# Optimization experiments

Measured on AMD Instinct MI355X. Metric: run time of the kernel, lower is better.

The kernel has to match this reference:

```python
import jax, jax.numpy as jnp
import numpy as np

N, E, IN_DIM, H_DIM, T = 100000, 3200000, 128, 128, 5000


def gcn_conv(x, W, b, src, dst):
    """PyG GCNConv: symmetric norm with self-loops, linear transform, scatter-add."""
    n = x.shape[0]
    h = x @ W  # [N, h]
    # degree with self-loops (all edge weights = 1)
    deg = jax.ops.segment_sum(jnp.ones(src.shape[0], x.dtype), dst, num_segments=n) + 1.0
    dinv = jax.lax.rsqrt(deg)  # deg >= 1 due to self-loops
    norm = dinv[src] * dinv[dst]  # [E]
    out = jax.ops.segment_sum(h[src] * norm[:, None], dst, num_segments=n)
    out = out + h * (dinv * dinv)[:, None]  # self-loop contribution
    return out + b


def setup_inputs() -> dict:
    key = jax.random.key(0)
    ks = jax.random.split(key, 24)
    s_in = 1.0 / np.sqrt(IN_DIM)
    s_h = 1.0 / np.sqrt(H_DIM)
    return {
        "x": jax.random.normal(ks[0], (N, IN_DIM), jnp.float32),
        "edge_index": jax.random.randint(ks[1], (2, E), 0, N),
        "fake_x": jax.random.normal(ks[2], (N, IN_DIM), jnp.float32),
        "fake_edge_index": jax.random.randint(ks[3], (2, E), 0, N),
        "treat_idx": jax.random.randint(ks[4], (T,), 0, N),
        "control_idx": jax.random.randint(ks[5], (T,), 0, N),
        # GCN layer params
        "W1": jax.random.normal(ks[6], (IN_DIM, H_DIM), jnp.float32) * s_in,
        "b1": jnp.zeros((H_DIM,), jnp.float32),
        "W2": jax.random.normal(ks[7], (H_DIM, H_DIM), jnp.float32) * s_h,
        "b2": jnp.zeros((H_DIM,), jnp.float32),
        # heads
        "Wy1": jax.random.normal(ks[8], (H_DIM, 1), jnp.float32) * s_h,
        "by1": jnp.zeros((1,), jnp.float32),
        "Wy0": jax.random.normal(ks[9], (H_DIM, 1), jnp.float32) * s_h,
        "by0": jnp.zeros((1,), jnp.float32),
        "Wb": jax.random.normal(ks[10], (H_DIM, 2), jnp.float32) * s_h,
        "bb": jnp.zeros((2,), jnp.float32),
        "Wp1": jax.random.normal(ks[11], (H_DIM, H_DIM), jnp.float32) * s_h,
        "bp1": jnp.zeros((H_DIM,), jnp.float32),
        "Wp2": jax.random.normal(ks[12], (H_DIM, 2), jnp.float32) * s_h,
        "bp2": jnp.zeros((2,), jnp.float32),
    }


@jax.custom_vjp
def grl(x):
    return x

def _grl_fwd(x):
    return x, None

def _grl_bwd(_, g):
    return (-g,)

grl.defvjp(_grl_fwd, _grl_bwd)


def reference(x, edge_index, fake_x, fake_edge_index, treat_idx, control_idx,
              W1, b1, W2, b2, Wy1, by1, Wy0, by0, Wb, bb, Wp1, bp1, Wp2, bp2):
    lrelu = jax.nn.leaky_relu  # slope 0.01 matches torch default
    src, dst = edge_index[0], edge_index[1]
    fsrc, fdst = fake_edge_index[0], fake_edge_index[1]

    # layer 1 + relu (dropout is identity in eval mode)
    xZ1 = jax.nn.relu(gcn_conv(x, W1, b1, src, dst))
    xfZ1 = jax.nn.relu(gcn_conv(fake_x, W1, b1, fsrc, fdst))
    # layer 2
    xZ2 = gcn_conv(xZ1, W2, b2, src, dst)
    xfZ2 = gcn_conv(xfZ1, W2, b2, fsrc, fdst)

    y1 = lrelu(xZ2[treat_idx] @ Wy1 + by1).squeeze(-1)
    yc0 = lrelu(xfZ2[treat_idx] @ Wy0 + by0).squeeze(-1)
    y0 = lrelu(xZ2[control_idx] @ Wy0 + by0).squeeze(-1)
    yc1 = lrelu(xfZ2[control_idx] @ Wy1 + by1).squeeze(-1)

    fprob = grl(xZ2) @ Wb + bb
    fprob_f = grl(xfZ2) @ Wb + bb

    tprob = lrelu(lrelu(xZ2 @ Wp1 + bp1) @ Wp2 + bp2)
    tprob_f = lrelu(lrelu(xfZ2 @ Wp1 + bp1) @ Wp2 + bp2)

    return (y1, yc0, y0, yc1, fprob, fprob_f, tprob, tprob_f)
```

## Files before the change

### kernel.cpp

```cpp
#include <hip/hip_runtime.h>

#define DIM 128
#define EPB 8192
#define BINSH 8
#define BINN 256

typedef unsigned int uint32;
typedef __attribute__((ext_vector_type(8))) short short8;
typedef __attribute__((ext_vector_type(4))) float f32x4;

__device__ __forceinline__ uint32 bf16_rtne(float f) {
  uint32 u = __float_as_uint(f);
  return (u + 0x7FFFu + ((u >> 16) & 1u)) >> 16;
}
__device__ __forceinline__ float bf16_to_f(uint32 h) { return __uint_as_float(h << 16); }
__device__ __forceinline__ void unpack2(uint32 u, float& x, float& y) {
  x = __uint_as_float(u << 16);
  y = __uint_as_float(u & 0xFFFF0000u);
}


__launch_bounds__(256)
__global__ void csr_sort_kernel(const int* __restrict__ src, const int* __restrict__ dst,
                                int E, int nb1, uint32* __restrict__ tmp,
                                int* __restrict__ dir) {
  __shared__ uint32 sorted[EPB];
  __shared__ int lcnt[512];
  __shared__ int lbase[512];
  __shared__ int ps[256];
  int t = threadIdx.x;
  int base = blockIdx.x * EPB;

  lcnt[t] = 0;
  lcnt[t + 256] = 0;
  __syncthreads();

  uint32 val[32];
  uint32 br[32];
#pragma unroll
  for (int i = 0; i < 32; ++i) {
    int e = base + i * 256 + t;
    if (e < E) {
      int d = __builtin_nontemporal_load(dst + e);
      int s = __builtin_nontemporal_load(src + e);
      int bin = d >> BINSH;
      val[i] = ((uint32)s << BINSH) | (uint32)(d & (BINN - 1));
      int rank = atomicAdd(&lcnt[bin], 1);
      br[i] = ((uint32)bin << 13) | (uint32)rank;
    } else {
      br[i] = 0xFFFFFFFFu;
    }
  }
  __syncthreads();

  {
    int a0 = lcnt[2 * t], a1 = lcnt[2 * t + 1];
    int psum = a0 + a1;
    ps[t] = psum;
    __syncthreads();
    for (int off = 1; off < 256; off <<= 1) {
      int x = (t >= off) ? ps[t - off] : 0;
      __syncthreads();
      ps[t] += x;
      __syncthreads();
    }
    int ebase = ps[t] - psum;
    lbase[2 * t] = ebase;
    lbase[2 * t + 1] = ebase + a0;
  }
  __syncthreads();

#pragma unroll
  for (int i = 0; i < 32; ++i) {
    if (br[i] != 0xFFFFFFFFu) {
      int bin = br[i] >> 13;
      int rank = br[i] & 0x1FFF;
      sorted[lbase[bin] + rank] = val[i];
    }
  }
  __syncthreads();

  int cnt = min(EPB, E - base);
#pragma unroll
  for (int i = 0; i < 32; ++i) {
    int idx = i * 256 + t;
    if (idx < cnt) tmp[base + idx] = sorted[idx];
  }
  for (int b = t; b <= nb1; b += 256) {
    dir[blockIdx.x * (nb1 + 1) + b] = lbase[b];
  }
}


__launch_bounds__(256)
__global__ void csr_build_kernel(const uint32* __restrict__ tmp, const int* __restrict__ dir,
                                 int nA, int nb1, int N, int binCap,
                                 int* __restrict__ row_beg, int* __restrict__ row_end,
                                 int* __restrict__ cols, float* __restrict__ dinv) {
  __shared__ int rbeg[512];
  __shared__ int rend[512];
  __shared__ int deg[BINN];
  __shared__ int cur[BINN];
  __shared__ int ps[256];
  int j = blockIdx.x;
  int t = threadIdx.x;
  int node0 = j << BINSH;
  int colsBase = j * binCap;

  if (t < BINN) deg[t] = 0;
  for (int i = t; i < nA; i += 256) {
    rbeg[i] = dir[i * (nb1 + 1) + j];
    rend[i] = dir[i * (nb1 + 1) + j + 1];
  }
  __syncthreads();

  for (int i = t; i < nA; i += 256) {
    int b = rbeg[i], en = rend[i];
    for (int q = b; q < en; ++q) {
      atomicAdd(&deg[tmp[(size_t)i * EPB + q] & (BINN - 1)], 1);
    }
  }
  __syncthreads();

  int dv = deg[t];
  ps[t] = dv;
  __syncthreads();
  for (int off = 1; off < 256; off <<= 1) {
    int x = (t >= off) ? ps[t - off] : 0;
    __syncthreads();
    ps[t] += x;
    __syncthreads();
  }
  int ebase = ps[t] - dv;
  cur[t] = ebase;
  int node = node0 + t;
  if (node < N) {
    row_beg[node] = colsBase + ebase;
    row_end[node] = colsBase + ebase + dv;
    dinv[node] = rsqrtf((float)dv + 1.0f);
  }
  __syncthreads();

  for (int i = t; i < nA; i += 256) {
    int b = rbeg[i], en = rend[i];
    for (int q = b; q < en; ++q) {
      uint32 v = tmp[(size_t)i * EPB + q];
      int p = atomicAdd(&cur[v & (BINN - 1)], 1);
      cols[colsBase + p] = (int)(v >> BINSH);
    }
  }
}


__global__ void wsplit_kernel(const float* __restrict__ W, uint4* __restrict__ hi4,
                              uint4* __restrict__ lo4) {
  int tid = blockIdx.x * blockDim.x + threadIdx.x;
  int lane = tid & 63;
  int ks = (tid >> 6) & 3;
  int ct = tid >> 8;
  int col = ct * 16 + (lane & 15);
  int k0 = ks * 32 + ((lane >> 4) << 3);
  uint32 h[8], l[8];
#pragma unroll
  for (int j = 0; j < 8; ++j) {
    float w = W[(size_t)(k0 + j) * DIM + col];
    uint32 hh = bf16_rtne(w);
    float rem = w - bf16_to_f(hh);
    l[j] = bf16_rtne(rem);
    h[j] = hh;
  }
  uint4 H, L;
  H.x = h[0] | (h[1] << 16); H.y = h[2] | (h[3] << 16);
  H.z = h[4] | (h[5] << 16); H.w = h[6] | (h[7] << 16);
  L.x = l[0] | (l[1] << 16); L.y = l[2] | (l[3] << 16);
  L.z = l[4] | (l[5] << 16); L.w = l[6] | (l[7] << 16);
  hi4[tid] = H;
  lo4[tid] = L;
}


__launch_bounds__(256, 3)
__global__ void gemm_mfma_kernel(const float* __restrict__ in, const uint4* __restrict__ wHi,
                                 const uint4* __restrict__ wLo, uint32* __restrict__ outb,
                                 int n, const float* __restrict__ rowscale,
                                 const float* __restrict__ bias, float slope, int in_bf16,
                                 const float* __restrict__ headW,
                                 const float* __restrict__ headB,
                                 float* __restrict__ headOut) {
  __shared__ unsigned short sA[2 * 64 * 128];
  __shared__ unsigned short sO[64 * 128];
  int t = threadIdx.x;
  int row0 = blockIdx.x * 64;

  if (in_bf16) {
    const uint4* in4 = (const uint4*)in;
    int q = t & 15;
    int rl = t >> 4;
#pragma unroll
    for (int i = 0; i < 4; ++i) {
      int row = rl + i * 16;
      int grow = row0 + row;
      uint4 v = make_uint4(0, 0, 0, 0);
      if (grow < n) v = in4[(size_t)grow * 16 + q];
      int sidx = (row * 128 + q * 8) ^ ((row & 7) << 3);
      *(uint4*)&sA[sidx] = v;
    }
  } else {
    int quad = t & 31;
    int r = t >> 5;
#pragma unroll
    for (int i = 0; i < 8; ++i) {
      int row = r + i * 8;
      int grow = row0 + row;
      f32x4 v = (f32x4){0.f, 0.f, 0.f, 0.f};
      if (grow < n) v = *(const f32x4*)(in + (size_t)grow * DIM + quad * 4);
      uint32 h0 = bf16_rtne(v.x), h1 = bf16_rtne(v.y), h2 = bf16_rtne(v.z), h3 = bf16_rtne(v.w);
      uint32 l0 = bf16_rtne(v.x - bf16_to_f(h0));
      uint32 l1 = bf16_rtne(v.y - bf16_to_f(h1));
      uint32 l2 = bf16_rtne(v.z - bf16_to_f(h2));
      uint32 l3 = bf16_rtne(v.w - bf16_to_f(h3));
      int sidx = (row * 128 + quad * 4) ^ ((row & 7) << 3);
      *(uint2*)&sA[sidx] = make_uint2(h0 | (h1 << 16), h2 | (h3 << 16));
      *(uint2*)&sA[64 * 128 + sidx] = make_uint2(l0 | (l1 << 16), l2 | (l3 << 16));
    }
  }
  __syncthreads();

  int lane = t & 63;
  int w = t >> 6;
  int rbase = w * 16;
  f32x4 acc[8];
#pragma unroll
  for (int ct = 0; ct < 8; ++ct) acc[ct] = (f32x4){0.f, 0.f, 0.f, 0.f};

  int fragRow = rbase + (lane & 15);
  int fragSwz = (fragRow & 7) << 3;
#pragma unroll
  for (int ks = 0; ks < 4; ++ks) {
    int cidx = ks * 32 + ((lane >> 4) << 3);
    int sidx = (fragRow * 128 + cidx) ^ fragSwz;
    uint4 au = *(uint4*)&sA[sidx];
    short8 ah = __builtin_bit_cast(short8, au);
    short8 al;
    if (!in_bf16) al = __builtin_bit_cast(short8, *(uint4*)&sA[64 * 128 + sidx]);
#pragma unroll
    for (int ct = 0; ct < 8; ++ct) {
      int widx = (ct * 4 + ks) * 64 + lane;
      short8 bh = __builtin_bit_cast(short8, wHi[widx]);
      short8 bl = __builtin_bit_cast(short8, wLo[widx]);
      if (!in_bf16) acc[ct] = __builtin_amdgcn_mfma_f32_16x16x32_bf16(al, bh, acc[ct], 0, 0, 0);
      acc[ct] = __builtin_amdgcn_mfma_f32_16x16x32_bf16(ah, bl, acc[ct], 0, 0, 0);
      acc[ct] = __builtin_amdgcn_mfma_f32_16x16x32_bf16(ah, bh, acc[ct], 0, 0, 0);
    }
  }

  float rs[4];
#pragma unroll
  for (int r = 0; r < 4; ++r) {
    int grow = row0 + rbase + ((lane >> 4) << 2) + r;
    rs[r] = rowscale ? ((grow < n) ? rowscale[grow] : 0.f) : 1.0f;
  }

  float hp0[4] = {0.f, 0.f, 0.f, 0.f};
  float hp1[4] = {0.f, 0.f, 0.f, 0.f};

#pragma unroll
  for (int ct = 0; ct < 8; ++ct) {
    int col = ct * 16 + (lane & 15);
    float bv = bias ? bias[col] : 0.f;
    float hw0 = 0.f, hw1 = 0.f;
    if (headOut) {
      hw0 = headW[col * 2 + 0];
      hw1 = headW[col * 2 + 1];
    }
#pragma unroll
    for (int r = 0; r < 4; ++r) {
      int rowL = rbase + ((lane >> 4) << 2) + r;
      float v = acc[ct][r] * rs[r] + bv;
      v = (v > 0.f) ? v : v * slope;
      if (outb) {
        int sidx = (rowL * 128 + col) ^ ((rowL & 7) << 3);
        sO[sidx] = (unsigned short)bf16_rtne(v);
      }
      if (headOut) {
        hp0[r] = fmaf(v, hw0, hp0[r]);
        hp1[r] = fmaf(v, hw1, hp1[r]);
      }
    }
  }

  if (headOut) {
    float hb0 = headB[0], hb1 = headB[1];
#pragma unroll
    for (int r = 0; r < 4; ++r) {
      float a = hp0[r], b = hp1[r];
#pragma unroll
      for (int off = 8; off; off >>= 1) {
        a += __shfl_xor(a, off);
        b += __shfl_xor(b, off);
      }
      if ((lane & 15) == 0) {
        int grow = row0 + rbase + ((lane >> 4) << 2) + r;
        if (grow < n) {
          float o0 = a + hb0, o1 = b + hb1;
          headOut[2 * (size_t)grow + 0] = (o0 > 0.f) ? o0 : 0.01f * o0;
          headOut[2 * (size_t)grow + 1] = (o1 > 0.f) ? o1 : 0.01f * o1;
        }
      }
    }
  }

  if (outb) {
    __syncthreads();
#pragma unroll
    for (int it = 0; it < 4; ++it) {
      int s = it * 64 + lane;
      int row = rbase + (s >> 4);
      int sin = s & 15;
      int sidx = row * 128 + ((sin * 8) ^ ((row & 7) << 3));
      uint4 v = *(uint4*)&sO[sidx];
      int grow = row0 + row;
      if (grow < n) *(uint4*)(outb + (size_t)grow * 64 + sin * 4) = v;
    }
  }
}


__launch_bounds__(256)
__global__ void agg_kernel(const uint32* __restrict__ g, const int* __restrict__ row_beg,
                           const int* __restrict__ row_end, const int* __restrict__ cols,
                           const float* __restrict__ dinv, const float* __restrict__ bias,
                           void* __restrict__ out, int n, int relu, int out_bf16,
                           const float* __restrict__ fpW, const float* __restrict__ fpB,
                           float* __restrict__ fpOut) {
  int lane = threadIdx.x & 63;
  int node = (blockIdx.x * blockDim.x + threadIdx.x) >> 6;
  if (node >= n) return;
  int beg = row_beg[node];
  int end = row_end[node];
  float ax, ay;
  unpack2(g[(size_t)node * 64 + lane], ax, ay);
  float bx = 0.f, by = 0.f;
  int e = beg;
  for (; e + 16 <= end; e += 16) {
    int s[16];
#pragma unroll
    for (int i = 0; i < 16; ++i) s[i] = cols[e + i];
    uint32 u[16];
#pragma unroll
    for (int i = 0; i < 16; ++i) u[i] = g[(size_t)s[i] * 64 + lane];
#pragma unroll
    for (int i = 0; i < 16; i += 2) {
      float x0, y0, x1, y1;
      unpack2(u[i], x0, y0);
      unpack2(u[i + 1], x1, y1);
      ax += x0; ay += y0;
      bx += x1; by += y1;
    }
  }
  if (e + 8 <= end) {
    int s[8];
#pragma unroll
    for (int i = 0; i < 8; ++i) s[i] = cols[e + i];
    uint32 u[8];
#pragma unroll
    for (int i = 0; i < 8; ++i) u[i] = g[(size_t)s[i] * 64 + lane];
#pragma unroll
    for (int i = 0; i < 8; i += 2) {
      float x0, y0, x1, y1;
      unpack2(u[i], x0, y0);
      unpack2(u[i + 1], x1, y1);
      ax += x0; ay += y0;
      bx += x1; by += y1;
    }
    e += 8;
  }
  for (; e < end; ++e) {
    uint32 u0 = g[(size_t)cols[e] * 64 + lane];
    float x0, y0;
    unpack2(u0, x0, y0);
    ax += x0;
    ay += y0;
  }
  ax += bx;
  ay += by;
  float di = dinv[node];
  float2 bv = ((const float2*)bias)[lane];
  float ox = fmaf(di, ax, bv.x);
  float oy = fmaf(di, ay, bv.y);
  if (relu) {
    ox = fmaxf(ox, 0.f);
    oy = fmaxf(oy, 0.f);
  }
  if (out_bf16) {
    uint32 pk = bf16_rtne(ox) | (bf16_rtne(oy) << 16);
    ((uint32*)out)[(size_t)node * 64 + lane] = pk;
  } else {
    ((float2*)out)[(size_t)node * 64 + lane] = make_float2(ox, oy);
  }

  if (fpOut) {
    float w00 = fpW[(2 * lane) * 2 + 0];
    float w01 = fpW[(2 * lane) * 2 + 1];
    float w10 = fpW[(2 * lane + 1) * 2 + 0];
    float w11 = fpW[(2 * lane + 1) * 2 + 1];
    float p0 = ox * w00 + oy * w10;
    float p1 = ox * w01 + oy * w11;
#pragma unroll
    for (int off = 32; off; off >>= 1) {
      p0 += __shfl_xor(p0, off);
      p1 += __shfl_xor(p1, off);
    }
    if (lane == 0) {
      fpOut[2 * (size_t)node + 0] = p0 + fpB[0];
      fpOut[2 * (size_t)node + 1] = p1 + fpB[1];
    }
  }
}


__global__ void ydot2_kernel(const uint32* __restrict__ Z,
                             const int* __restrict__ idxA, const float* __restrict__ wA,
                             const float* __restrict__ bA, float* __restrict__ outA,
                             const int* __restrict__ idxB, const float* __restrict__ wB,
                             const float* __restrict__ bB, float* __restrict__ outB,
                             int T) {
  int lane = threadIdx.x & 63;
  int t = (blockIdx.x * blockDim.x + threadIdx.x) >> 6;
  if (t >= 2 * T) return;
  int isB = (t >= T);
  int ti = isB ? (t - T) : t;
  const int* idx = isB ? idxB : idxA;
  const float* w = isB ? wB : wA;
  const float* b = isB ? bB : bA;
  float* o = isB ? outB : outA;
  float2 wv = ((const float2*)w)[lane];
  int node = idx[ti];
  float zx, zy;
  unpack2(Z[(size_t)node * 64 + lane], zx, zy);
  float pp = zx * wv.x + zy * wv.y;
#pragma unroll
  for (int off = 32; off; off >>= 1) pp += __shfl_xor(pp, off);
  if (lane == 0) {
    float v = pp + b[0];
    o[ti] = (v > 0.f) ? v : 0.01f * v;
  }
}


extern "C" void kernel_launch(void* const* d_in, const int* in_sizes, int n_in,
                              void* d_out, int out_size, void* d_ws, size_t ws_size,
                              hipStream_t stream) {
  const int N = in_sizes[0] / DIM;
  const int E = in_sizes[1] / 2;
  const int T = in_sizes[4];
  const int nb1 = (N + BINN - 1) >> BINSH;
  const int nA = (E + EPB - 1) / EPB;
  const int binCap = ((E / nb1 + 1024 + 15) / 16) * 16;

  const float* x = (const float*)d_in[0];
  const int* ei = (const int*)d_in[1];
  const float* fx = (const float*)d_in[2];
  const int* fei = (const int*)d_in[3];
  const int* treat = (const int*)d_in[4];
  const int* control = (const int*)d_in[5];
  const float* W1 = (const float*)d_in[6];
  const float* b1 = (const float*)d_in[7];
  const float* W2 = (const float*)d_in[8];
  const float* b2 = (const float*)d_in[9];
  const float* Wy1 = (const float*)d_in[10];
  const float* by1 = (const float*)d_in[11];
  const float* Wy0 = (const float*)d_in[12];
  const float* by0 = (const float*)d_in[13];
  const float* Wb = (const float*)d_in[14];
  const float* bb = (const float*)d_in[15];
  const float* Wp1 = (const float*)d_in[16];
  const float* bp1 = (const float*)d_in[17];
  const float* Wp2 = (const float*)d_in[18];
  const float* bp2 = (const float*)d_in[19];

  float* out = (float*)d_out;

  char* p = (char*)d_ws;
  float* bufZ = (float*)p;   p += (size_t)N * DIM * sizeof(float);
  uint32* bufG = (uint32*)p; p += (size_t)N * (DIM / 2) * sizeof(uint32);
  int* cols = (int*)p;       p += (size_t)nb1 * binCap * sizeof(int);
  int* dir = (int*)p;        p += (size_t)nA * (nb1 + 1) * sizeof(int);
  int* row_beg = (int*)p;    p += (size_t)(N + 16) * sizeof(int);
  int* row_end = (int*)p;    p += (size_t)(N + 16) * sizeof(int);
  float* dinv = (float*)p;   p += (size_t)(N + 16) * sizeof(float);
  uint4* w1Hi = (uint4*)p;   p += 2048 * sizeof(uint4);
  uint4* w1Lo = (uint4*)p;   p += 2048 * sizeof(uint4);
  uint4* w2Hi = (uint4*)p;   p += 2048 * sizeof(uint4);
  uint4* w2Lo = (uint4*)p;   p += 2048 * sizeof(uint4);
  uint4* wp1Hi = (uint4*)p;  p += 2048 * sizeof(uint4);
  uint4* wp1Lo = (uint4*)p;  p += 2048 * sizeof(uint4);
  uint32* tmp = (uint32*)bufZ;

  float* oy1 = out;
  float* oyc0 = out + T;
  float* oy0 = out + 2 * T;
  float* oyc1 = out + 3 * T;
  float* ofp = out + 4 * T;
  float* ofpf = out + 4 * T + 2 * N;
  float* otp = out + 4 * T + 4 * N;
  float* otpf = out + 4 * T + 6 * N;

  wsplit_kernel<<<8, 256, 0, stream>>>(W1, w1Hi, w1Lo);
  wsplit_kernel<<<8, 256, 0, stream>>>(W2, w2Hi, w2Lo);
  wsplit_kernel<<<8, 256, 0, stream>>>(Wp1, wp1Hi, wp1Lo);

  auto run = [&](const float* X, const int* EI,
                 float* y_t, const float* Wt, const float* bt,
                 float* y_c, const float* Wc, const float* bc,
                 float* fp, float* tp) {
    const int* srcp = EI;
    const int* dstp = EI + E;
    csr_sort_kernel<<<nA, 256, 0, stream>>>(srcp, dstp, E, nb1, tmp, dir);
    csr_build_kernel<<<nb1, 256, 0, stream>>>(tmp, dir, nA, nb1, N, binCap,
                                              row_beg, row_end, cols, dinv);
    gemm_mfma_kernel<<<(N + 63) / 64, 256, 0, stream>>>(X, w1Hi, w1Lo, bufG, N, dinv,
                                                        nullptr, 1.0f, 0, nullptr, nullptr, nullptr);
    agg_kernel<<<(N + 3) / 4, 256, 0, stream>>>(bufG, row_beg, row_end, cols, dinv, b1,
                                                (void*)bufZ, N, 1, 1, nullptr, nullptr, nullptr);
    gemm_mfma_kernel<<<(N + 63) / 64, 256, 0, stream>>>(bufZ, w2Hi, w2Lo, bufG, N, dinv,
                                                        nullptr, 1.0f, 1, nullptr, nullptr, nullptr);
    agg_kernel<<<(N + 3) / 4, 256, 0, stream>>>(bufG, row_beg, row_end, cols, dinv, b2,
                                                (void*)bufZ, N, 0, 1, Wb, bb, fp);
    gemm_mfma_kernel<<<(N + 63) / 64, 256, 0, stream>>>(bufZ, wp1Hi, wp1Lo, nullptr, N, nullptr,
                                                        bp1, 0.01f, 1, Wp2, bp2, tp);
    ydot2_kernel<<<(2 * T + 3) / 4, 256, 0, stream>>>((const uint32*)bufZ,
                                                      treat, Wt, bt, y_t,
                                                      control, Wc, bc, y_c, T);
  };

  run(x, ei, oy1, Wy1, by1, oy0, Wy0, by0, ofp, otp);
  run(fx, fei, oyc0, Wy0, by0, oyc1, Wy1, by1, ofpf, otpf);
}
```

Baseline: 862.6 us.

## Gather neighbor rows with 16-byte loads across four edge groups per wavefront

The aggregation kernel now splits each 64-lane wavefront into four 16-lane groups. Each group loads one whole bf16 neighbor row using uint4 vector loads, so four edges are processed at once, and the partial sums are reduced with cross-lane shuffles. This cuts the number of memory instructions per edge and raises the number of independent gathers in flight. The cost is more registers, shuffle reductions, and idle lanes on the final store. The three weight-split launches are also merged into a single kernel launch.

After: 849.0 us. No clear change (-1.6%).

```diff
diff --git a/kernel.cpp b/kernel.cpp
--- a/kernel.cpp
+++ b/kernel.cpp
@@ -14,6 +14,8 @@
   return (u + 0x7FFFu + ((u >> 16) & 1u)) >> 16;
 }
 __device__ __forceinline__ float bf16_to_f(uint32 h) { return __uint_as_float(h << 16); }
+__device__ __forceinline__ float lo16f(uint32 u) { return __uint_as_float(u << 16); }
+__device__ __forceinline__ float hi16f(uint32 u) { return __uint_as_float(u & 0xFFFF0000u); }
 __device__ __forceinline__ void unpack2(uint32 u, float& x, float& y) {
   x = __uint_as_float(u << 16);
   y = __uint_as_float(u & 0xFFFF0000u);
@@ -152,9 +154,14 @@
 }
 
 
-__global__ void wsplit_kernel(const float* __restrict__ W, uint4* __restrict__ hi4,
-                              uint4* __restrict__ lo4) {
-  int tid = blockIdx.x * blockDim.x + threadIdx.x;
+__global__ void wsplit3_kernel(const float* __restrict__ Wa, uint4* __restrict__ hiA, uint4* __restrict__ loA,
+                               const float* __restrict__ Wb, uint4* __restrict__ hiB, uint4* __restrict__ loB,
+                               const float* __restrict__ Wc, uint4* __restrict__ hiC, uint4* __restrict__ loC) {
+  int widx = blockIdx.x >> 3;
+  int tid = (blockIdx.x & 7) * 256 + threadIdx.x;
+  const float* W = (widx == 0) ? Wa : (widx == 1) ? Wb : Wc;
+  uint4* hi4 = (widx == 0) ? hiA : (widx == 1) ? hiB : hiC;
+  uint4* lo4 = (widx == 0) ? loA : (widx == 1) ? loB : loC;
   int lane = tid & 63;
   int ks = (tid >> 6) & 3;
   int ct = tid >> 8;
@@ -330,84 +337,85 @@
 __global__ void agg_kernel(const uint32* __restrict__ g, const int* __restrict__ row_beg,
                            const int* __restrict__ row_end, const int* __restrict__ cols,
                            const float* __restrict__ dinv, const float* __restrict__ bias,
-                           void* __restrict__ out, int n, int relu, int out_bf16,
+                           uint32* __restrict__ out, int n, int relu,
                            const float* __restrict__ fpW, const float* __restrict__ fpB,
                            float* __restrict__ fpOut) {
   int lane = threadIdx.x & 63;
   int node = (blockIdx.x * blockDim.x + threadIdx.x) >> 6;
   if (node >= n) return;
-  int beg = row_beg[node];
-  int end = row_end[node];
-  float ax, ay;
-  unpack2(g[(size_t)node * 64 + lane], ax, ay);
-  float bx = 0.f, by = 0.f;
+  int grp = lane >> 4;
+  int p = lane & 15;
+  int beg = row_beg[node], end = row_end[node];
+  const uint4* __restrict__ g4 = (const uint4*)g;
+
+  float acc[8];
+#pragma unroll
+  for (int j = 0; j < 8; ++j) acc[j] = 0.f;
+
   int e = beg;
-  for (; e + 16 <= end; e += 16) {
-    int s[16];
-#pragma unroll
-    for (int i = 0; i < 16; ++i) s[i] = cols[e + i];
-    uint32 u[16];
-#pragma unroll
-    for (int i = 0; i < 16; ++i) u[i] = g[(size_t)s[i] * 64 + lane];
-#pragma unroll
-    for (int i = 0; i < 16; i += 2) {
-      float x0, y0, x1, y1;
-      unpack2(u[i], x0, y0);
-      unpack2(u[i + 1], x1, y1);
-      ax += x0; ay += y0;
-      bx += x1; by += y1;
-    }
-  }
-  if (e + 8 <= end) {
-    int s[8];
-#pragma unroll
-    for (int i = 0; i < 8; ++i) s[i] = cols[e + i];
-    uint32 u[8];
-#pragma unroll
-    for (int i = 0; i < 8; ++i) u[i] = g[(size_t)s[i] * 64 + lane];
-#pragma unroll
-    for (int i = 0; i < 8; i += 2) {
-      float x0, y0, x1, y1;
-      unpack2(u[i], x0, y0);
-      unpack2(u[i + 1], x1, y1);
-      ax += x0; ay += y0;
-      bx += x1; by += y1;
-    }
-    e += 8;
-  }
-  for (; e < end; ++e) {
-    uint32 u0 = g[(size_t)cols[e] * 64 + lane];
-    float x0, y0;
-    unpack2(u0, x0, y0);
-    ax += x0;
-    ay += y0;
-  }
-  ax += bx;
-  ay += by;
+  for (; e + 8 <= end; e += 8) {
+    int c0 = cols[e + grp];
+    int c1 = cols[e + 4 + grp];
+    uint4 v0 = g4[(size_t)c0 * 16 + p];
+    uint4 v1 = g4[(size_t)c1 * 16 + p];
+    acc[0] += lo16f(v0.x); acc[1] += hi16f(v0.x);
+    acc[2] += lo16f(v0.y); acc[3] += hi16f(v0.y);
+    acc[4] += lo16f(v0.z); acc[5] += hi16f(v0.z);
+    acc[6] += lo16f(v0.w); acc[7] += hi16f(v0.w);
+    acc[0] += lo16f(v1.x); acc[1] += hi16f(v1.x);
+    acc[2] += lo16f(v1.y); acc[3] += hi16f(v1.y);
+    acc[4] += lo16f(v1.z); acc[5] += hi16f(v1.z);
+    acc[6] += lo16f(v1.w); acc[7] += hi16f(v1.w);
+  }
+  for (; e < end; e += 4) {
+    int idx = e + grp;
+    if (idx < end) {
+      int c = cols[idx];
+      uint4 v = g4[(size_t)c * 16 + p];
+      acc[0] += lo16f(v.x); acc[1] += hi16f(v.x);
+      acc[2] += lo16f(v.y); acc[3] += hi16f(v.y);
+      acc[4] += lo16f(v.z); acc[5] += hi16f(v.z);
+      acc[6] += lo16f(v.w); acc[7] += hi16f(v.w);
+    }
+  }
+
+#pragma unroll
+  for (int j = 0; j < 8; ++j) {
+    acc[j] += __shfl_xor(acc[j], 16);
+    acc[j] += __shfl_xor(acc[j], 32);
+  }
+
+  {
+    uint4 sv = g4[(size_t)node * 16 + p];
+    acc[0] += lo16f(sv.x); acc[1] += hi16f(sv.x);
+    acc[2] += lo16f(sv.y); acc[3] += hi16f(sv.y);
+    acc[4] += lo16f(sv.z); acc[5] += hi16f(sv.z);
+    acc[6] += lo16f(sv.w); acc[7] += hi16f(sv.w);
+  }
+
   float di = dinv[node];
-  float2 bv = ((const float2*)bias)[lane];
-  float ox = fmaf(di, ax, bv.x);
-  float oy = fmaf(di, ay, bv.y);
+  const float4* b4 = (const float4*)bias;
+  float4 bv0 = b4[2 * p], bv1 = b4[2 * p + 1];
+  float o[8];
+  o[0] = fmaf(di, acc[0], bv0.x); o[1] = fmaf(di, acc[1], bv0.y);
+  o[2] = fmaf(di, acc[2], bv0.z); o[3] = fmaf(di, acc[3], bv0.w);
+  o[4] = fmaf(di, acc[4], bv1.x); o[5] = fmaf(di, acc[5], bv1.y);
+  o[6] = fmaf(di, acc[6], bv1.z); o[7] = fmaf(di, acc[7], bv1.w);
   if (relu) {
-    ox = fmaxf(ox, 0.f);
-    oy = fmaxf(oy, 0.f);
-  }
-  if (out_bf16) {
-    uint32 pk = bf16_rtne(ox) | (bf16_rtne(oy) << 16);
-    ((uint32*)out)[(size_t)node * 64 + lane] = pk;
-  } else {
-    ((float2*)out)[(size_t)node * 64 + lane] = make_float2(ox, oy);
+#pragma unroll
+    for (int j = 0; j < 8; ++j) o[j] = fmaxf(o[j], 0.f);
   }
 
   if (fpOut) {
-    float w00 = fpW[(2 * lane) * 2 + 0];
-    float w01 = fpW[(2 * lane) * 2 + 1];
-    float w10 = fpW[(2 * lane + 1) * 2 + 0];
-    float w11 = fpW[(2 * lane + 1) * 2 + 1];
-    float p0 = ox * w00 + oy * w10;
-    float p1 = ox * w01 + oy * w11;
-#pragma unroll
-    for (int off = 32; off; off >>= 1) {
+    float p0 = 0.f, p1 = 0.f;
+#pragma unroll
+    for (int j = 0; j < 8; ++j) {
+      int col = p * 8 + j;
+      p0 = fmaf(o[j], fpW[col * 2 + 0], p0);
+      p1 = fmaf(o[j], fpW[col * 2 + 1], p1);
+    }
+#pragma unroll
+    for (int off = 8; off; off >>= 1) {
       p0 += __shfl_xor(p0, off);
       p1 += __shfl_xor(p1, off);
     }
@@ -415,6 +423,15 @@
       fpOut[2 * (size_t)node + 0] = p0 + fpB[0];
       fpOut[2 * (size_t)node + 1] = p1 + fpB[1];
     }
+  }
+
+  if (grp == 0) {
+    uint4 pk;
+    pk.x = bf16_rtne(o[0]) | (bf16_rtne(o[1]) << 16);
+    pk.y = bf16_rtne(o[2]) | (bf16_rtne(o[3]) << 16);
+    pk.z = bf16_rtne(o[4]) | (bf16_rtne(o[5]) << 16);
+    pk.w = bf16_rtne(o[6]) | (bf16_rtne(o[7]) << 16);
+    ((uint4*)out)[(size_t)node * 16 + p] = pk;
   }
 }
 
@@ -506,9 +523,7 @@
   float* otp = out + 4 * T + 4 * N;
   float* otpf = out + 4 * T + 6 * N;
 
-  wsplit_kernel<<<8, 256, 0, stream>>>(W1, w1Hi, w1Lo);
-  wsplit_kernel<<<8, 256, 0, stream>>>(W2, w2Hi, w2Lo);
-  wsplit_kernel<<<8, 256, 0, stream>>>(Wp1, wp1Hi, wp1Lo);
+  wsplit3_kernel<<<24, 256, 0, stream>>>(W1, w1Hi, w1Lo, W2, w2Hi, w2Lo, Wp1, wp1Hi, wp1Lo);
 
   auto run = [&](const float* X, const int* EI,
                  float* y_t, const float* Wt, const float* bt,
@@ -522,11 +537,11 @@
     gemm_mfma_kernel<<<(N + 63) / 64, 256, 0, stream>>>(X, w1Hi, w1Lo, bufG, N, dinv,
                                                         nullptr, 1.0f, 0, nullptr, nullptr, nullptr);
     agg_kernel<<<(N + 3) / 4, 256, 0, stream>>>(bufG, row_beg, row_end, cols, dinv, b1,
-                                                (void*)bufZ, N, 1, 1, nullptr, nullptr, nullptr);
+                                                (uint32*)bufZ, N, 1, nullptr, nullptr, nullptr);
     gemm_mfma_kernel<<<(N + 63) / 64, 256, 0, stream>>>(bufZ, w2Hi, w2Lo, bufG, N, dinv,
                                                         nullptr, 1.0f, 1, nullptr, nullptr, nullptr);
     agg_kernel<<<(N + 3) / 4, 256, 0, stream>>>(bufG, row_beg, row_end, cols, dinv, b2,
-                                                (void*)bufZ, N, 0, 1, Wb, bb, fp);
+                                                (uint32*)bufZ, N, 0, Wb, bb, fp);
     gemm_mfma_kernel<<<(N + 63) / 64, 256, 0, stream>>>(bufZ, wp1Hi, wp1Lo, nullptr, N, nullptr,
                                                         bp1, 0.01f, 1, Wp2, bp2, tp);
     ydot2_kernel<<<(2 * T + 3) / 4, 256, 0, stream>>>((const uint32*)bufZ,
```
